# Performance work log

Hardware: AMD Instinct MI355X
Metric: run time of the kernel (lower is better)

The kernel has to match this reference:

```python
import jax, jax.numpy as jnp
import numpy as np

B, N, D, K = 4, 4096, 64, 16
SCALE = float(np.sqrt(D))


def setup_inputs() -> dict:
    key = jax.random.key(0)
    ks = jax.random.split(key, 16)
    f = lambda i, shape: jax.random.normal(ks[i], shape, dtype=jnp.float32) * 0.05
    return {
        'x': jax.random.normal(ks[0], (B, N, D), dtype=jnp.float32),
        'pos': jax.random.uniform(ks[1], (B, N, 3), dtype=jnp.float32),
        'Wq': f(2, (D, D)), 'Wk': f(3, (D, D)), 'Wv': f(4, (D, D)),
        'P1': f(5, (3, D)), 'p1b': f(6, (D,)), 'P2': f(7, (D, D)), 'p2b': f(8, (D,)),
        'A1': f(9, (D, D)), 'a1b': f(10, (D,)), 'A2': f(11, (D, D)), 'a2b': f(12, (D,)),
        'Wf': f(13, (D, D)), 'bf': f(14, (D,)),
    }


def _gather(feats, idx):
    # feats: [B,N,C], idx: [B,N,K] -> [B,N,K,C]  (index_points / idx_pt)
    return jax.vmap(lambda f, i: f[i])(feats, idx)


def reference(x, pos, Wq, Wk, Wv, P1, p1b, P2, p2b, A1, a1b, A2, a2b, Wf, bf):
    # kNN via squared distances (same math as square_distance + argsort[:, :, :k])
    sq = jnp.sum(pos * pos, axis=-1)                                   # [B,N]
    dists = sq[:, :, None] + sq[:, None, :] - 2.0 * jnp.einsum('bnc,bmc->bnm', pos, pos)
    _, idx = jax.lax.top_k(-dists, K)                                  # [B,N,K]

    knn_xyz = _gather(pos, idx)                                        # [B,N,K,3]
    q = x @ Wq                                                         # [B,N,D]
    kf = _gather(x @ Wk, idx)                                          # [B,N,K,D]
    v = _gather(x @ Wv, idx)                                           # [B,N,K,D]

    rel = pos[:, :, None, :] - knn_xyz                                 # [B,N,K,3]
    pos_enc = jax.nn.relu(rel @ P1 + p1b) @ P2 + p2b                   # [B,N,K,D]

    attn = jax.nn.relu((q[:, :, None, :] - kf + pos_enc) @ A1 + a1b) @ A2 + a2b
    attn = jax.nn.softmax(attn / SCALE, axis=-2)                       # softmax over K

    agg = jnp.sum(attn * (v + pos_enc), axis=2)                        # [B,N,D]
    return agg @ Wf + bf + x                                           # residual
```

## Files before the change

kernel.cpp:

```cpp
#include <hip/hip_runtime.h>
#include <hip/hip_bf16.h>
#include <stdint.h>

#define B_ 4
#define N_ 4096
#define D_ 64
#define K_ 16

static const size_t OFS_WQA1  = 0;
static const size_t OFS_WKA1  = 4096;
static const size_t OFS_WCOMB = 8192;
static const size_t OFS_C1    = 16384;
static const size_t OFS_QA1   = 16448;
static const size_t OFS_KA1   = OFS_QA1 + (size_t)B_*N_*64;
static const size_t OFS_V     = OFS_KA1 + (size_t)B_*N_*64;
static const size_t OFS_IDX   = OFS_V   + (size_t)B_*N_*64;
static const size_t OFS_POS4  = OFS_IDX + (size_t)B_*N_*16;
static const size_t OFS_BF16  = OFS_POS4 + (size_t)B_*N_*4;
static const size_t OFS_PBF   = OFS_BF16 + 6144;
static const size_t OFS_WFB   = OFS_PBF + 6144;

typedef __attribute__((ext_vector_type(8))) short short8;
typedef __attribute__((ext_vector_type(4))) float floatx4;

__device__ __forceinline__ unsigned short f2bf(float f) {
    __hip_bfloat16 h = __float2bfloat16(f);
    return *reinterpret_cast<unsigned short*>(&h);
}

__device__ __forceinline__ unsigned long long bsortu64(unsigned long long v, int l) {
#pragma unroll
    for (int k = 2; k <= 64; k <<= 1) {
#pragma unroll
        for (int j = k >> 1; j > 0; j >>= 1) {
            unsigned long long o = __shfl_xor(v, j, 64);
            unsigned long long mn = v < o ? v : o;
            unsigned long long mx = v < o ? o : v;
            v = ((((l & j) == 0) == ((l & k) == 0))) ? mn : mx;
        }
    }
    return v;
}

__device__ __forceinline__ void bsortu64x2(unsigned long long& a, unsigned long long& b, int l) {
#pragma unroll
    for (int k = 2; k <= 64; k <<= 1) {
#pragma unroll
        for (int j = k >> 1; j > 0; j >>= 1) {
            unsigned long long oa = __shfl_xor(a, j, 64);
            unsigned long long ob = __shfl_xor(b, j, 64);
            bool up = (((l & j) == 0) == ((l & k) == 0));
            unsigned long long mna = a < oa ? a : oa, mxa = a < oa ? oa : a;
            unsigned long long mnb = b < ob ? b : ob, mxb = b < ob ? ob : b;
            a = up ? mna : mxa;
            b = up ? mnb : mxb;
        }
    }
}

__global__ __launch_bounds__(256) void k_pre(
        const float* __restrict__ Wq, const float* __restrict__ Wk,
        const float* __restrict__ Wv, const float* __restrict__ Wf,
        const float* __restrict__ P2, const float* __restrict__ A1,
        const float* __restrict__ p2b, const float* __restrict__ a1b,
        const float* __restrict__ pos, float* __restrict__ ws) {
    int blk = blockIdx.x;
    unsigned short* pbf = (unsigned short*)(ws + OFS_PBF);
    if (blk < 65) {
        int i = blk * 256 + threadIdx.x;
        if (i < 4096) {
            int c = i >> 6, d = i & 63;
            float s = 0.f;
            for (int e = 0; e < 64; ++e) s = fmaf(Wq[c*64+e], A1[e*64+d], s);
            ws[OFS_WQA1 + i] = s;
            pbf[d*64 + c] = f2bf(s);
        } else if (i < 8192) {
            int j = i - 4096; int c = j >> 6, d = j & 63;
            float s = 0.f;
            for (int e = 0; e < 64; ++e) s = fmaf(Wk[c*64+e], A1[e*64+d], s);
            ws[OFS_WKA1 + j] = s;
            pbf[(64+d)*64 + c] = f2bf(s);
        } else if (i < 16384) {
            int j = i - 8192; int c = j >> 7, dd = j & 127;
            float s;
            if (dd < 64) { s = 0.f; for (int e = 0; e < 64; ++e) s = fmaf(P2[c*64+e], A1[e*64+dd], s); }
            else s = P2[c*64 + (dd - 64)];
            ws[OFS_WCOMB + j] = s;
        } else if (i < 16448) {
            int d = i - 16384;
            float s = a1b[d];
            for (int e = 0; e < 64; ++e) s = fmaf(p2b[e], A1[e*64+d], s);
            ws[OFS_C1 + d] = s;
        }
    } else if (blk < 81) {
        int i = (blk - 65) * 256 + threadIdx.x;
        int c = i >> 6, d = i & 63;
        pbf[(128+d)*64 + c] = f2bf(Wv[c*64+d]);
    } else if (blk < 97) {
        int i = (blk - 81) * 256 + threadIdx.x;
        int c = i >> 6, d = i & 63;
        ((unsigned short*)(ws + OFS_WFB))[d*64 + c] = f2bf(Wf[c*64+d]);
    } else {
        int i = (blk - 97) * 256 + threadIdx.x;
        float px = pos[(size_t)i*3+0], py = pos[(size_t)i*3+1], pz = pos[(size_t)i*3+2];
        float sq = fmaf(pz, pz, fmaf(py, py, px*px));
        ((float4*)(ws + OFS_POS4))[i] = make_float4(px, py, pz, sq);
    }
}

__global__ __launch_bounds__(256) void k_projm(const float* __restrict__ x,
                                               const float* __restrict__ A2,
                                               float* __restrict__ ws) {
    __shared__ unsigned short xT[64*72];
    __shared__ unsigned short wTs[192*72];
    const int t = threadIdx.x;
    if (blockIdx.x >= 256) {
        int i = ((int)blockIdx.x - 256) * 256 + t;
        unsigned short* wbf = (unsigned short*)(ws + OFS_BF16);
        if (i < 8192) {
            int c = i >> 7, dd = i & 127;
            wbf[dd*64 + c] = f2bf(ws[OFS_WCOMB + i]);
        } else {
            int j = i - 8192; int e = j >> 6, d = j & 63;
            wbf[8192 + d*64 + e] = f2bf(A2[j]);
        }
        return;
    }
    const unsigned short* pbf = (const unsigned short*)(ws + OFS_PBF);
    const int g0 = (int)blockIdx.x * 64;

#pragma unroll
    for (int k = 0; k < 6; ++k) {
        int id  = t + 256*k;
        int row = id >> 3, cir = id & 7;
        uint4 vv = *(const uint4*)(pbf + row*64 + cir*8);
        *(uint4*)&wTs[row*72 + cir*8] = vv;
    }
    {
        int r = t >> 2, qd = t & 3;
        const float* src = x + (size_t)(g0 + r)*64 + qd*16;
        unsigned short hb[16];
#pragma unroll
        for (int u = 0; u < 16; ++u) hb[u] = f2bf(src[u]);
        *(uint4*)&xT[r*72 + qd*16]     = *(uint4*)&hb[0];
        *(uint4*)&xT[r*72 + qd*16 + 8] = *(uint4*)&hb[8];
    }
    __syncthreads();

    const int w = t >> 6, l = t & 63, lr = l & 15, q = l >> 4;
    floatx4 acc[12];
#pragma unroll
    for (int j = 0; j < 12; ++j) acc[j] = (floatx4){0.f, 0.f, 0.f, 0.f};
#pragma unroll
    for (int kb = 0; kb < 2; ++kb) {
        short8 a = *(const short8*)&xT[(16*w + lr)*72 + 32*kb + 8*q];
#pragma unroll
        for (int j = 0; j < 12; ++j) {
            short8 bfr = *(const short8*)&wTs[(16*j + lr)*72 + 32*kb + 8*q];
            acc[j] = __builtin_amdgcn_mfma_f32_16x16x32_bf16(a, bfr, acc[j], 0, 0, 0);
        }
    }
    float* qA1 = ws + OFS_QA1;
    float* kA1 = ws + OFS_KA1;
    float* vws = ws + OFS_V;
#pragma unroll
    for (int j = 0; j < 12; ++j) {
        int col = 16*j + lr;
        float* dst = (col < 64) ? qA1 : (col < 128 ? kA1 : vws);
        int c2 = col & 63;
#pragma unroll
        for (int r = 0; r < 4; ++r) {
            int grow = g0 + 16*w + 4*q + r;
            dst[(size_t)grow*64 + c2] = acc[j][r];
        }
    }
}

__global__ __launch_bounds__(512) void k_knn(float* __restrict__ ws) {
    __shared__ float4 tile[2048];
    __shared__ unsigned long long sbuf[16*128];
    const float4* pos4 = (const float4*)(ws + OFS_POS4);
    int* idx = (int*)(ws + OFS_IDX);
    const int t = threadIdx.x;
    const int l = t & 63, wv = t >> 6;
    const int b = (int)(blockIdx.x >> 8);
    const int q0 = ((int)(blockIdx.x & 255)) * 16 + 2*wv;
    const size_t g0r = (size_t)b * N_ + q0;
    const float4* pb = pos4 + (size_t)b * N_;

    float4 qa = pos4[g0r];
    float4 qb = pos4[g0r + 1];
    float d0[32], d1[32];
    float mn0 = 1e30f, mn1 = 1e30f;

#pragma unroll
    for (int i = 0; i < 4; ++i) tile[t + 512*i] = pb[t + 512*i];
    __syncthreads();
#pragma unroll 8
    for (int i = 0; i < 32; ++i) {
        float4 cd = tile[i*64 + l];
        float dotA = fmaf(qa.z, cd.z, fmaf(qa.y, cd.y, qa.x*cd.x));
        float dA = fmaxf(fmaf(-2.f, dotA, qa.w + cd.w), 0.f);
        float dotB = fmaf(qb.z, cd.z, fmaf(qb.y, cd.y, qb.x*cd.x));
        float dB = fmaxf(fmaf(-2.f, dotB, qb.w + cd.w), 0.f);
        d0[i] = dA; d1[i] = dB;
        mn0 = fminf(mn0, dA); mn1 = fminf(mn1, dB);
    }
    __syncthreads();
#pragma unroll
    for (int i = 0; i < 4; ++i) tile[t + 512*i] = pb[2048 + t + 512*i];
    __syncthreads();
#pragma unroll 8
    for (int i = 0; i < 32; ++i) {
        float4 cd = tile[i*64 + l];
        float dotA = fmaf(qa.z, cd.z, fmaf(qa.y, cd.y, qa.x*cd.x));
        mn0 = fminf(mn0, fmaxf(fmaf(-2.f, dotA, qa.w + cd.w), 0.f));
        float dotB = fmaf(qb.z, cd.z, fmaf(qb.y, cd.y, qb.x*cd.x));
        mn1 = fminf(mn1, fmaxf(fmaf(-2.f, dotB, qb.w + cd.w), 0.f));
    }

    float v0 = mn0, v1 = mn1;
#pragma unroll
    for (int k = 2; k <= 64; k <<= 1) {
#pragma unroll
        for (int j = k >> 1; j > 0; j >>= 1) {
            float o0 = __shfl_xor(v0, j, 64);
            float o1 = __shfl_xor(v1, j, 64);
            bool up = (((l & j) == 0) == ((l & k) == 0));
            v0 = up ? fminf(v0, o0) : fmaxf(v0, o0);
            v1 = up ? fminf(v1, o1) : fmaxf(v1, o1);
        }
    }
    float tau0 = __shfl(v0, 15, 64);
    float tau1 = __shfl(v1, 15, 64);

    unsigned long long* sb0 = sbuf + wv*256;
    unsigned long long* sb1 = sb0 + 128;
    const unsigned long long lmask = (1ull << l) - 1ull;
    int cnt0 = 0, cnt1 = 0;
#pragma unroll 8
    for (int i = 0; i < 32; ++i) {
        bool p0 = (d0[i] <= tau0);
        unsigned long long m0 = __ballot(p0);
        if (p0) {
            int pp = cnt0 + __popcll(m0 & lmask);
            if (pp < 128)
                sb0[pp] = ((unsigned long long)__float_as_uint(d0[i]) << 32) | (unsigned)(i*64 + l);
        }
        cnt0 += (int)__popcll(m0);
        bool p1 = (d1[i] <= tau1);
        unsigned long long m1 = __ballot(p1);
        if (p1) {
            int pp = cnt1 + __popcll(m1 & lmask);
            if (pp < 128)
                sb1[pp] = ((unsigned long long)__float_as_uint(d1[i]) << 32) | (unsigned)(i*64 + l);
        }
        cnt1 += (int)__popcll(m1);
    }
#pragma unroll 4
    for (int i = 0; i < 32; ++i) {
        float4 cd = tile[i*64 + l];
        float dotA = fmaf(qa.z, cd.z, fmaf(qa.y, cd.y, qa.x*cd.x));
        float dA = fmaxf(fmaf(-2.f, dotA, qa.w + cd.w), 0.f);
        float dotB = fmaf(qb.z, cd.z, fmaf(qb.y, cd.y, qb.x*cd.x));
        float dB = fmaxf(fmaf(-2.f, dotB, qb.w + cd.w), 0.f);
        bool p0 = (dA <= tau0);
        unsigned long long m0 = __ballot(p0);
        if (p0) {
            int pp = cnt0 + __popcll(m0 & lmask);
            if (pp < 128)
                sb0[pp] = ((unsigned long long)__float_as_uint(dA) << 32) | (unsigned)(2048 + i*64 + l);
        }
        cnt0 += (int)__popcll(m0);
        bool p1 = (dB <= tau1);
        unsigned long long m1 = __ballot(p1);
        if (p1) {
            int pp = cnt1 + __popcll(m1 & lmask);
            if (pp < 128)
                sb1[pp] = ((unsigned long long)__float_as_uint(dB) << 32) | (unsigned)(2048 + i*64 + l);
        }
        cnt1 += (int)__popcll(m1);
    }
    if (cnt0 > 128) cnt0 = 128;
    if (cnt1 > 128) cnt1 = 128;

    unsigned long long pk0 = (l < cnt0) ? sb0[l] : ~0ull;
    unsigned long long pk1 = (l < cnt1) ? sb1[l] : ~0ull;
    bsortu64x2(pk0, pk1, l);
    if (cnt0 > 64) {
        unsigned long long w2 = (64 + l < cnt0) ? sb0[64 + l] : ~0ull;
        w2 = bsortu64(w2, l);
        unsigned long long bb = __shfl(w2, (l - 16) & 63, 64);
        unsigned long long nv = (l < 16) ? pk0 : ((l < 32) ? bb : ~0ull);
        pk0 = bsortu64(nv, l);
    }
    if (cnt1 > 64) {
        unsigned long long w2 = (64 + l < cnt1) ? sb1[64 + l] : ~0ull;
        w2 = bsortu64(w2, l);
        unsigned long long bb = __shfl(w2, (l - 16) & 63, 64);
        unsigned long long nv = (l < 16) ? pk1 : ((l < 32) ? bb : ~0ull);
        pk1 = bsortu64(nv, l);
    }
    if (l < 16) {
        idx[g0r*16 + l]       = (int)(pk0 & 0xffffffffu);
        idx[(g0r + 1)*16 + l] = (int)(pk1 & 0xffffffffu);
    }
}

__global__ __launch_bounds__(256) void k_attn(
    const float* __restrict__ x, const float* __restrict__ pos,
    const float* __restrict__ P1, const float* __restrict__ p1b,
    const float* __restrict__ p2b, const float* __restrict__ a2b,
    const float* __restrict__ bff, const float* __restrict__ ws,
    float* __restrict__ out) {

    __shared__ unsigned short wT[128*72];
    __shared__ unsigned short a2T[64*72];
    __shared__ unsigned short abuf[128*72];
    __shared__ float relb[128*4];
    __shared__ int   mrow[128];

    const int t  = threadIdx.x;
    const int g0 = blockIdx.x * 8;
    const int b  = g0 >> 12;
    const float* qA1 = ws + OFS_QA1;
    const float* kA1 = ws + OFS_KA1;
    const float* vws = ws + OFS_V;
    const float* c1  = ws + OFS_C1;
    const int* idx = (const int*)(ws + OFS_IDX);
    const unsigned short* wbf = (const unsigned short*)(ws + OFS_BF16);
    const unsigned short* wfb = (const unsigned short*)(ws + OFS_WFB);

#pragma unroll
    for (int k = 0; k < 6; ++k) {
        int id  = t + 256*k;
        int row = id >> 3, cir = id & 7;
        uint4 vv = *(const uint4*)(wbf + row*64 + cir*8);
        if (row < 128) *(uint4*)&wT[row*72 + cir*8] = vv;
        else           *(uint4*)&a2T[(row-128)*72 + cir*8] = vv;
    }

    if (t < 128) {
        int p = t >> 4, k = t & 15;
        int ng = g0 + p;
        int m  = idx[(size_t)ng*16 + k];
        int mg = b * N_ + m;
        mrow[t] = mg;
        relb[t*4+0] = pos[(size_t)ng*3+0] - pos[(size_t)mg*3+0];
        relb[t*4+1] = pos[(size_t)ng*3+1] - pos[(size_t)mg*3+1];
        relb[t*4+2] = pos[(size_t)ng*3+2] - pos[(size_t)mg*3+2];
    }
    __syncthreads();

    const int w = t >> 6, l = t & 63, lr = l & 15, q = l >> 4;

    float kpre[2][4][4];
    float qpre[2][4];
#pragma unroll
    for (int i = 0; i < 2; ++i) {
        int ng = g0 + 2*w + i;
#pragma unroll
        for (int j = 0; j < 4; ++j) {
            int col = 16*j + lr;
            qpre[i][j] = qA1[(size_t)ng*64 + col] + c1[col];
#pragma unroll
            for (int r = 0; r < 4; ++r) {
                int row = 32*w + 16*i + 4*q + r;
                kpre[i][j][r] = kA1[(size_t)mrow[row]*64 + col];
            }
        }
    }

    {
        int d = t & 63, r0 = t >> 6;
        float w0 = P1[d], w1 = P1[64+d], w2 = P1[128+d], bb = p1b[d];
#pragma unroll
        for (int jj = 0; jj < 32; ++jj) {
            int r = r0 + jj*4;
            float h = fmaf(relb[r*4+2], w2, fmaf(relb[r*4+1], w1, fmaf(relb[r*4+0], w0, bb)));
            abuf[r*72 + d] = f2bf(fmaxf(h, 0.f));
        }
    }
    __syncthreads();

    floatx4 acc1[2][8];
#pragma unroll
    for (int i = 0; i < 2; ++i)
#pragma unroll
        for (int j = 0; j < 8; ++j) acc1[i][j] = (floatx4){0.f, 0.f, 0.f, 0.f};
#pragma unroll
    for (int kb = 0; kb < 2; ++kb) {
        short8 a0 = *(const short8*)&abuf[(32*w      + lr)*72 + 32*kb + 8*q];
        short8 a1 = *(const short8*)&abuf[(32*w + 16 + lr)*72 + 32*kb + 8*q];
#pragma unroll
        for (int j = 0; j < 8; ++j) {
            short8 bfr = *(const short8*)&wT[(16*j + lr)*72 + 32*kb + 8*q];
            acc1[0][j] = __builtin_amdgcn_mfma_f32_16x16x32_bf16(a0, bfr, acc1[0][j], 0, 0, 0);
            acc1[1][j] = __builtin_amdgcn_mfma_f32_16x16x32_bf16(a1, bfr, acc1[1][j], 0, 0, 0);
        }
    }
    __syncthreads();

#pragma unroll
    for (int i = 0; i < 2; ++i) {
#pragma unroll
        for (int j = 0; j < 4; ++j) {
            int col = 16*j + lr;
            float qv = qpre[i][j];
#pragma unroll
            for (int r = 0; r < 4; ++r) {
                int row = 32*w + 16*i + 4*q + r;
                float t1 = acc1[i][j][r] + qv - kpre[i][j][r];
                abuf[row*72 + col] = f2bf(fmaxf(t1, 0.f));
            }
        }
    }

    float vpre[2][4][4];
#pragma unroll
    for (int i = 0; i < 2; ++i)
#pragma unroll
        for (int j = 0; j < 4; ++j) {
            int col = 16*j + lr;
#pragma unroll
            for (int r = 0; r < 4; ++r) {
                int row = 32*w + 16*i + 4*q + r;
                vpre[i][j][r] = vws[(size_t)mrow[row]*64 + col];
            }
        }
    short8 wffrag[2];
#pragma unroll
    for (int kb = 0; kb < 2; ++kb)
        wffrag[kb] = *(const short8*)&wfb[(16*w + lr)*64 + 32*kb + 8*q];
    __syncthreads();

    floatx4 acc2[2][4];
#pragma unroll
    for (int i = 0; i < 2; ++i)
#pragma unroll
        for (int j = 0; j < 4; ++j) acc2[i][j] = (floatx4){0.f, 0.f, 0.f, 0.f};
#pragma unroll
    for (int kb = 0; kb < 2; ++kb) {
        short8 a0 = *(const short8*)&abuf[(32*w      + lr)*72 + 32*kb + 8*q];
        short8 a1 = *(const short8*)&abuf[(32*w + 16 + lr)*72 + 32*kb + 8*q];
#pragma unroll
        for (int j = 0; j < 4; ++j) {
            short8 bfr = *(const short8*)&a2T[(16*j + lr)*72 + 32*kb + 8*q];
            acc2[0][j] = __builtin_amdgcn_mfma_f32_16x16x32_bf16(a0, bfr, acc2[0][j], 0, 0, 0);
            acc2[1][j] = __builtin_amdgcn_mfma_f32_16x16x32_bf16(a1, bfr, acc2[1][j], 0, 0, 0);
        }
    }
    __syncthreads();

#pragma unroll
    for (int i = 0; i < 2; ++i) {
#pragma unroll
        for (int j = 0; j < 4; ++j) {
            int col = 16*j + lr;
            float a2bv = a2b[col], p2bv = p2b[col];
            float L[4];
#pragma unroll
            for (int r = 0; r < 4; ++r) L[r] = acc2[i][j][r] + a2bv;
            float mx = fmaxf(fmaxf(L[0], L[1]), fmaxf(L[2], L[3]));
            mx = fmaxf(mx, __shfl_xor(mx, 16, 64));
            mx = fmaxf(mx, __shfl_xor(mx, 32, 64));
            float ssum = 0.f, part = 0.f;
#pragma unroll
            for (int r = 0; r < 4; ++r) {
                float e = __expf((L[r] - mx) * 0.125f);
                ssum += e;
                float wv = vpre[i][j][r] + (acc1[i][4+j][r] + p2bv);
                part = fmaf(e, wv, part);
            }
            ssum += __shfl_xor(ssum, 16, 64);
            ssum += __shfl_xor(ssum, 32, 64);
            part += __shfl_xor(part, 16, 64);
            part += __shfl_xor(part, 32, 64);
            float agg = part / ssum;
            if (q == 0) abuf[(2*w + i)*72 + col] = f2bf(agg);
        }
    }
    __syncthreads();

    {
        floatx4 accF = (floatx4){0.f, 0.f, 0.f, 0.f};
#pragma unroll
        for (int kb = 0; kb < 2; ++kb) {
            short8 afr = *(const short8*)&abuf[lr*72 + 32*kb + 8*q];
            accF = __builtin_amdgcn_mfma_f32_16x16x32_bf16(afr, wffrag[kb], accF, 0, 0, 0);
        }
        if (q < 2) {
            int col = 16*w + lr;
            float bv = bff[col];
#pragma unroll
            for (int r = 0; r < 4; ++r) {
                int g = g0 + 4*q + r;
                out[(size_t)g*64 + col] = accF[r] + bv + x[(size_t)g*64 + col];
            }
        }
    }
}

extern "C" void kernel_launch(void* const* d_in, const int* in_sizes, int n_in,
                              void* d_out, int out_size, void* d_ws, size_t ws_size,
                              hipStream_t stream) {
    const float* x   = (const float*)d_in[0];
    const float* pos = (const float*)d_in[1];
    const float* Wq  = (const float*)d_in[2];
    const float* Wk  = (const float*)d_in[3];
    const float* Wv  = (const float*)d_in[4];
    const float* P1  = (const float*)d_in[5];
    const float* p1b = (const float*)d_in[6];
    const float* P2  = (const float*)d_in[7];
    const float* p2b = (const float*)d_in[8];
    const float* A1  = (const float*)d_in[9];
    const float* a1b = (const float*)d_in[10];
    const float* A2  = (const float*)d_in[11];
    const float* a2b = (const float*)d_in[12];
    const float* Wf  = (const float*)d_in[13];
    const float* bf  = (const float*)d_in[14];
    float* out = (float*)d_out;
    float* ws  = (float*)d_ws;

    hipLaunchKernelGGL(k_pre,   dim3(161),  dim3(256), 0, stream,
                       Wq, Wk, Wv, Wf, P2, A1, p2b, a1b, pos, ws);
    hipLaunchKernelGGL(k_projm, dim3(304),  dim3(256), 0, stream, x, A2, ws);
    hipLaunchKernelGGL(k_knn,   dim3(1024), dim3(512), 0, stream, ws);
    hipLaunchKernelGGL(k_attn,  dim3(2048), dim3(256), 0, stream,
                       x, pos, P1, p1b, p2b, a2b, bf, ws, out);
}
```

Before: 169.2 us.

## Compute kNN distances with bf16 MFMA split-precision and threshold filtering

```diff
diff --git a/kernel.cpp b/kernel.cpp
--- a/kernel.cpp
+++ b/kernel.cpp
@@ -19,6 +19,10 @@
 static const size_t OFS_BF16  = OFS_POS4 + (size_t)B_*N_*4;
 static const size_t OFS_PBF   = OFS_BF16 + 6144;
 static const size_t OFS_WFB   = OFS_PBF + 6144;
+static const size_t OFS_APK   = OFS_WFB + 2048;
+static const size_t OFS_BPK   = OFS_APK + 262144;
+
+#define KNN_CAP 96
 
 typedef __attribute__((ext_vector_type(8))) short short8;
 typedef __attribute__((ext_vector_type(4))) float floatx4;
@@ -26,6 +30,11 @@
 __device__ __forceinline__ unsigned short f2bf(float f) {
     __hip_bfloat16 h = __float2bfloat16(f);
     return *reinterpret_cast<unsigned short*>(&h);
+}
+
+__device__ __forceinline__ float bf2f(unsigned short u) {
+    __hip_bfloat16 h = *reinterpret_cast<__hip_bfloat16*>(&u);
+    return __bfloat162float(h);
 }
 
 __device__ __forceinline__ unsigned long long bsortu64(unsigned long long v, int l) {
@@ -105,6 +114,28 @@
         float px = pos[(size_t)i*3+0], py = pos[(size_t)i*3+1], pz = pos[(size_t)i*3+2];
         float sq = fmaf(pz, pz, fmaf(py, py, px*px));
         ((float4*)(ws + OFS_POS4))[i] = make_float4(px, py, pz, sq);
+
+        unsigned short xh = f2bf(px), yh = f2bf(py), zh = f2bf(pz), sh = f2bf(sq);
+        float xl = px - bf2f(xh), yl = py - bf2f(yh), zl = pz - bf2f(zh), sl = sq - bf2f(sh);
+        unsigned short xlb = f2bf(xl), ylb = f2bf(yl), zlb = f2bf(zl), slb = f2bf(sl);
+        unsigned short m2xh = f2bf(-2.f*bf2f(xh)), m2yh = f2bf(-2.f*bf2f(yh)), m2zh = f2bf(-2.f*bf2f(zh));
+        unsigned short m2xl = f2bf(-2.f*xl), m2yl = f2bf(-2.f*yl), m2zl = f2bf(-2.f*zl);
+        const unsigned short ONE = 0x3F80;
+        union { unsigned short u[32]; uint4 v[4]; } A, Bp;
+#pragma unroll
+        for (int j2 = 0; j2 < 32; ++j2) { A.u[j2] = 0; Bp.u[j2] = 0; }
+        A.u[0]=m2xh; A.u[1]=m2xh; A.u[2]=m2xl;
+        A.u[3]=m2yh; A.u[4]=m2yh; A.u[5]=m2yl;
+        A.u[6]=m2zh; A.u[7]=m2zh; A.u[8]=m2zl;
+        A.u[9]=sh;   A.u[10]=slb; A.u[11]=ONE; A.u[12]=ONE;
+        Bp.u[0]=xh;  Bp.u[1]=xlb; Bp.u[2]=xh;
+        Bp.u[3]=yh;  Bp.u[4]=ylb; Bp.u[5]=yh;
+        Bp.u[6]=zh;  Bp.u[7]=zlb; Bp.u[8]=zh;
+        Bp.u[9]=ONE; Bp.u[10]=ONE; Bp.u[11]=sh; Bp.u[12]=slb;
+        uint4* ap4 = (uint4*)(ws + OFS_APK);
+        uint4* bp4 = (uint4*)(ws + OFS_BPK);
+#pragma unroll
+        for (int j2 = 0; j2 < 4; ++j2) { ap4[(size_t)i*4+j2] = A.v[j2]; bp4[(size_t)i*4+j2] = Bp.v[j2]; }
     }
 }
 
@@ -176,134 +207,135 @@
     }
 }
 
-__global__ __launch_bounds__(512) void k_knn(float* __restrict__ ws) {
-    __shared__ float4 tile[2048];
-    __shared__ unsigned long long sbuf[16*128];
-    const float4* pos4 = (const float4*)(ws + OFS_POS4);
-    int* idx = (int*)(ws + OFS_IDX);
-    const int t = threadIdx.x;
-    const int l = t & 63, wv = t >> 6;
-    const int b = (int)(blockIdx.x >> 8);
-    const int q0 = ((int)(blockIdx.x & 255)) * 16 + 2*wv;
-    const size_t g0r = (size_t)b * N_ + q0;
-    const float4* pb = pos4 + (size_t)b * N_;
-
-    float4 qa = pos4[g0r];
-    float4 qb = pos4[g0r + 1];
-    float d0[32], d1[32];
-    float mn0 = 1e30f, mn1 = 1e30f;
-
-#pragma unroll
-    for (int i = 0; i < 4; ++i) tile[t + 512*i] = pb[t + 512*i];
-    __syncthreads();
-#pragma unroll 8
-    for (int i = 0; i < 32; ++i) {
-        float4 cd = tile[i*64 + l];
-        float dotA = fmaf(qa.z, cd.z, fmaf(qa.y, cd.y, qa.x*cd.x));
-        float dA = fmaxf(fmaf(-2.f, dotA, qa.w + cd.w), 0.f);
-        float dotB = fmaf(qb.z, cd.z, fmaf(qb.y, cd.y, qb.x*cd.x));
-        float dB = fmaxf(fmaf(-2.f, dotB, qb.w + cd.w), 0.f);
-        d0[i] = dA; d1[i] = dB;
-        mn0 = fminf(mn0, dA); mn1 = fminf(mn1, dB);
-    }
-    __syncthreads();
-#pragma unroll
-    for (int i = 0; i < 4; ++i) tile[t + 512*i] = pb[2048 + t + 512*i];
-    __syncthreads();
-#pragma unroll 8
-    for (int i = 0; i < 32; ++i) {
-        float4 cd = tile[i*64 + l];
-        float dotA = fmaf(qa.z, cd.z, fmaf(qa.y, cd.y, qa.x*cd.x));
-        mn0 = fminf(mn0, fmaxf(fmaf(-2.f, dotA, qa.w + cd.w), 0.f));
-        float dotB = fmaf(qb.z, cd.z, fmaf(qb.y, cd.y, qb.x*cd.x));
-        mn1 = fminf(mn1, fmaxf(fmaf(-2.f, dotB, qb.w + cd.w), 0.f));
-    }
-
-    float v0 = mn0, v1 = mn1;
-#pragma unroll
-    for (int k = 2; k <= 64; k <<= 1) {
-#pragma unroll
-        for (int j = k >> 1; j > 0; j >>= 1) {
-            float o0 = __shfl_xor(v0, j, 64);
-            float o1 = __shfl_xor(v1, j, 64);
-            bool up = (((l & j) == 0) == ((l & k) == 0));
-            v0 = up ? fminf(v0, o0) : fmaxf(v0, o0);
-            v1 = up ? fminf(v1, o1) : fmaxf(v1, o1);
-        }
-    }
-    float tau0 = __shfl(v0, 15, 64);
-    float tau1 = __shfl(v1, 15, 64);
-
-    unsigned long long* sb0 = sbuf + wv*256;
-    unsigned long long* sb1 = sb0 + 128;
-    const unsigned long long lmask = (1ull << l) - 1ull;
-    int cnt0 = 0, cnt1 = 0;
-#pragma unroll 8
-    for (int i = 0; i < 32; ++i) {
-        bool p0 = (d0[i] <= tau0);
-        unsigned long long m0 = __ballot(p0);
-        if (p0) {
-            int pp = cnt0 + __popcll(m0 & lmask);
-            if (pp < 128)
-                sb0[pp] = ((unsigned long long)__float_as_uint(d0[i]) << 32) | (unsigned)(i*64 + l);
-        }
-        cnt0 += (int)__popcll(m0);
-        bool p1 = (d1[i] <= tau1);
-        unsigned long long m1 = __ballot(p1);
-        if (p1) {
-            int pp = cnt1 + __popcll(m1 & lmask);
-            if (pp < 128)
-                sb1[pp] = ((unsigned long long)__float_as_uint(d1[i]) << 32) | (unsigned)(i*64 + l);
-        }
-        cnt1 += (int)__popcll(m1);
-    }
-#pragma unroll 4
-    for (int i = 0; i < 32; ++i) {
-        float4 cd = tile[i*64 + l];
-        float dotA = fmaf(qa.z, cd.z, fmaf(qa.y, cd.y, qa.x*cd.x));
-        float dA = fmaxf(fmaf(-2.f, dotA, qa.w + cd.w), 0.f);
-        float dotB = fmaf(qb.z, cd.z, fmaf(qb.y, cd.y, qb.x*cd.x));
-        float dB = fmaxf(fmaf(-2.f, dotB, qb.w + cd.w), 0.f);
-        bool p0 = (dA <= tau0);
-        unsigned long long m0 = __ballot(p0);
-        if (p0) {
-            int pp = cnt0 + __popcll(m0 & lmask);
-            if (pp < 128)
-                sb0[pp] = ((unsigned long long)__float_as_uint(dA) << 32) | (unsigned)(2048 + i*64 + l);
-        }
-        cnt0 += (int)__popcll(m0);
-        bool p1 = (dB <= tau1);
-        unsigned long long m1 = __ballot(p1);
-        if (p1) {
-            int pp = cnt1 + __popcll(m1 & lmask);
-            if (pp < 128)
-                sb1[pp] = ((unsigned long long)__float_as_uint(dB) << 32) | (unsigned)(2048 + i*64 + l);
-        }
-        cnt1 += (int)__popcll(m1);
-    }
-    if (cnt0 > 128) cnt0 = 128;
-    if (cnt1 > 128) cnt1 = 128;
-
-    unsigned long long pk0 = (l < cnt0) ? sb0[l] : ~0ull;
-    unsigned long long pk1 = (l < cnt1) ? sb1[l] : ~0ull;
-    bsortu64x2(pk0, pk1, l);
-    if (cnt0 > 64) {
-        unsigned long long w2 = (64 + l < cnt0) ? sb0[64 + l] : ~0ull;
+__device__ __forceinline__ unsigned long long knn_pack_entry(
+        const float4 q4, const float4* __restrict__ pos4b,
+        const unsigned* s0, const unsigned* s1, int c0, int T, int e) {
+    bool valid = e < T;
+    int i0 = (e < c0) ? e : 0;
+    int i1 = e - c0; i1 = i1 < 0 ? 0 : (i1 > KNN_CAP-1 ? KNN_CAP-1 : i1);
+    unsigned idxv = (e < c0) ? s0[i0] : s1[i1];
+    idxv = valid ? (idxv & 4095u) : 0u;
+    float4 c4 = pos4b[idxv];
+    float dot = fmaf(q4.z, c4.z, fmaf(q4.y, c4.y, q4.x*c4.x));
+    float d = fmaxf(fmaf(-2.f, dot, q4.w + c4.w), 0.f);
+    unsigned long long pk = ((unsigned long long)__float_as_uint(d) << 32) | idxv;
+    return valid ? pk : ~0ull;
+}
+
+__device__ __forceinline__ unsigned long long knn_merge_rest(
+        unsigned long long best, int l, const float4 q4,
+        const float4* __restrict__ pos4b,
+        const unsigned* s0, const unsigned* s1, int c0, int T) {
+    for (int base = 64; base < T; base += 64) {
+        unsigned long long w2 = knn_pack_entry(q4, pos4b, s0, s1, c0, T, base + l);
         w2 = bsortu64(w2, l);
         unsigned long long bb = __shfl(w2, (l - 16) & 63, 64);
-        unsigned long long nv = (l < 16) ? pk0 : ((l < 32) ? bb : ~0ull);
-        pk0 = bsortu64(nv, l);
-    }
-    if (cnt1 > 64) {
-        unsigned long long w2 = (64 + l < cnt1) ? sb1[64 + l] : ~0ull;
-        w2 = bsortu64(w2, l);
-        unsigned long long bb = __shfl(w2, (l - 16) & 63, 64);
-        unsigned long long nv = (l < 16) ? pk1 : ((l < 32) ? bb : ~0ull);
-        pk1 = bsortu64(nv, l);
-    }
-    if (l < 16) {
-        idx[g0r*16 + l]       = (int)(pk0 & 0xffffffffu);
-        idx[(g0r + 1)*16 + l] = (int)(pk1 & 0xffffffffu);
+        unsigned long long nv = (l < 16) ? best : ((l < 32) ? bb : ~0ull);
+        best = bsortu64(nv, l);
+    }
+    return best;
+}
+
+__global__ __launch_bounds__(256) void k_knn(float* __restrict__ ws) {
+    __shared__ unsigned surv[32*2*KNN_CAP];
+    __shared__ int scnt[64];
+    const unsigned short* apk = (const unsigned short*)(ws + OFS_APK);
+    const unsigned short* bpk = (const unsigned short*)(ws + OFS_BPK);
+    const int t = threadIdx.x;
+    const int w = t >> 6, l = t & 63;
+    const int grp = w >> 1, hf = w & 1;
+    const int lr = l & 15, hi4 = l >> 4;
+    const int g0 = (int)blockIdx.x * 32;
+    const int b  = g0 >> 12;
+
+    short8 afrag = *(const short8*)(apk + (size_t)(g0 + grp*16 + lr)*32 + 8*hi4);
+    const unsigned short* bbase = bpk + (size_t)(b*4096 + hf*2048 + lr)*32 + 8*hi4;
+    const floatx4 z4 = {0.f, 0.f, 0.f, 0.f};
+
+    float run1[4], run2[4];
+#pragma unroll
+    for (int r = 0; r < 4; ++r) { run1[r] = 1e30f; run2[r] = 1e30f; }
+#pragma unroll 4
+    for (int tt = 0; tt < 128; ++tt) {
+        short8 bfr = *(const short8*)(bbase + tt*512);
+        floatx4 a = __builtin_amdgcn_mfma_f32_16x16x32_bf16(afrag, bfr, z4, 0, 0, 0);
+#pragma unroll
+        for (int r = 0; r < 4; ++r) {
+            run2[r] = fminf(run2[r], fmaxf(run1[r], a[r]));
+            run1[r] = fminf(run1[r], a[r]);
+        }
+    }
+
+    float tau[4];
+#pragma unroll
+    for (int r = 0; r < 4; ++r) {
+        float v = run2[r];
+#pragma unroll
+        for (int k = 2; k <= 16; k <<= 1) {
+#pragma unroll
+            for (int j = k >> 1; j > 0; j >>= 1) {
+                float o = __shfl_xor(v, j, 64);
+                bool up = (((lr & j) == 0) == ((lr & k) == 0));
+                v = up ? fminf(v, o) : fmaxf(v, o);
+            }
+        }
+        tau[r] = __shfl(v, (l & 48) | 7, 64) + 1e-3f;
+    }
+
+    int cnt[4] = {0, 0, 0, 0};
+    const unsigned lm16 = (1u << lr) - 1u;
+    unsigned su[4];
+#pragma unroll
+    for (int r = 0; r < 4; ++r) su[r] = (unsigned)(((grp*16 + 4*hi4 + r)*2 + hf) * KNN_CAP);
+    const unsigned cand0 = (unsigned)(hf*2048 + lr);
+#pragma unroll 4
+    for (int tt = 0; tt < 128; ++tt) {
+        short8 bfr = *(const short8*)(bbase + tt*512);
+        floatx4 a = __builtin_amdgcn_mfma_f32_16x16x32_bf16(afrag, bfr, z4, 0, 0, 0);
+        unsigned cid = cand0 + (unsigned)(tt*16);
+#pragma unroll
+        for (int r = 0; r < 4; ++r) {
+            bool pred = a[r] <= tau[r];
+            unsigned long long m = __ballot(pred);
+            if (m) {
+                unsigned gm = (unsigned)(m >> (hi4 * 16)) & 0xFFFFu;
+                int pos = cnt[r] + __popc(gm & lm16);
+                if (pred && pos < KNN_CAP) surv[su[r] + pos] = cid;
+                cnt[r] += __popc(gm);
+            }
+        }
+    }
+    if (lr == 0) {
+#pragma unroll
+        for (int r = 0; r < 4; ++r) scnt[(grp*16 + 4*hi4 + r)*2 + hf] = cnt[r];
+    }
+    __syncthreads();
+
+    const float4* pos4g = (const float4*)(ws + OFS_POS4);
+    const float4* pos4b = pos4g + (size_t)b * N_;
+    int* idx = (int*)(ws + OFS_IDX);
+    for (int p = 0; p < 4; ++p) {
+        int qa = w*8 + 2*p, qb = qa + 1;
+        int c0a = scnt[qa*2+0]; c0a = c0a < KNN_CAP ? c0a : KNN_CAP;
+        int c1a = scnt[qa*2+1]; c1a = c1a < KNN_CAP ? c1a : KNN_CAP;
+        int c0b = scnt[qb*2+0]; c0b = c0b < KNN_CAP ? c0b : KNN_CAP;
+        int c1b = scnt[qb*2+1]; c1b = c1b < KNN_CAP ? c1b : KNN_CAP;
+        int Ta = c0a + c1a, Tb = c0b + c1b;
+        const unsigned* s0a = surv + (qa*2+0)*KNN_CAP;
+        const unsigned* s1a = surv + (qa*2+1)*KNN_CAP;
+        const unsigned* s0b = surv + (qb*2+0)*KNN_CAP;
+        const unsigned* s1b = surv + (qb*2+1)*KNN_CAP;
+        float4 q4a = pos4g[g0 + qa];
+        float4 q4b = pos4g[g0 + qb];
+        unsigned long long pk0 = knn_pack_entry(q4a, pos4b, s0a, s1a, c0a, Ta, l);
+        unsigned long long pk1 = knn_pack_entry(q4b, pos4b, s0b, s1b, c0b, Tb, l);
+        bsortu64x2(pk0, pk1, l);
+        if (Ta > 64) pk0 = knn_merge_rest(pk0, l, q4a, pos4b, s0a, s1a, c0a, Ta);
+        if (Tb > 64) pk1 = knn_merge_rest(pk1, l, q4b, pos4b, s0b, s1b, c0b, Tb);
+        if (l < 16) {
+            idx[(size_t)(g0 + qa)*16 + l] = (int)(pk0 & 0xFFFu);
+            idx[(size_t)(g0 + qb)*16 + l] = (int)(pk1 & 0xFFFu);
+        }
     }
 }
 
@@ -525,7 +557,7 @@
     hipLaunchKernelGGL(k_pre,   dim3(161),  dim3(256), 0, stream,
                        Wq, Wk, Wv, Wf, P2, A1, p2b, a1b, pos, ws);
     hipLaunchKernelGGL(k_projm, dim3(304),  dim3(256), 0, stream, x, A2, ws);
-    hipLaunchKernelGGL(k_knn,   dim3(1024), dim3(512), 0, stream, ws);
+    hipLaunchKernelGGL(k_knn,   dim3(512),  dim3(256), 0, stream, ws);
     hipLaunchKernelGGL(k_attn,  dim3(2048), dim3(256), 0, stream,
                        x, pos, P1, p1b, p2b, a2b, bf, ws, out);
 }
```

After: 206.2 us. 21.9% more time.
